# Kernel optimization log

Hardware: AMD Instinct MI355X
Metric: run time of the kernel (lower is better)

The kernel has to match this reference:

```python
import jax, jax.numpy as jnp
import numpy as np

N, E, D_IN, H, NSEG, SEG = 40000, 640000, 127, 128, 512, 64
D0 = D_IN + 1  # node features + batch-indicator column


def setup_inputs() -> dict:
    ks = jax.random.split(jax.random.key(0), 12)
    def w(k, i, o):
        return jax.random.normal(k, (i, o), jnp.float32) / np.float32(np.sqrt(i))
    return dict(
        x=jax.random.normal(ks[0], (N, D_IN), jnp.float32),
        ei=jax.random.randint(ks[1], (2, E), 0, N, jnp.int32),
        ew=jax.random.uniform(ks[2], (E,), jnp.float32),
        batches=jax.random.randint(ks[3], (NSEG * SEG,), 0, N, jnp.int32),
        lens=jnp.arange(NSEG + 1, dtype=jnp.int32) * SEG,  # CSR offsets, 512 segments of 64
        gin_w0=w(ks[4], D0, H), gin_b0=jnp.zeros((H,), jnp.float32),
        gin_w1=w(ks[5], H, H), gin_b1=jnp.zeros((H,), jnp.float32),
        gin_w2=w(ks[6], H, H), gin_b2=jnp.zeros((H,), jnp.float32),
        r_w1=w(ks[7], 3 * H, H), r_b1=jnp.zeros((H,), jnp.float32),
        ln1_g=jnp.ones((H,), jnp.float32), ln1_b=jnp.zeros((H,), jnp.float32),
        r_w2=w(ks[8], H, H), r_b2=jnp.zeros((H,), jnp.float32),
        ln2_g=jnp.ones((H,), jnp.float32), ln2_b=jnp.zeros((H,), jnp.float32),
        r_w3=w(ks[9], H, 1), r_b3=jnp.zeros((1,), jnp.float32),
    )


def _layernorm(v, g, b, eps=1e-5):
    m = jnp.mean(v, -1, keepdims=True)
    var = jnp.mean((v - m) ** 2, -1, keepdims=True)
    return (v - m) * jax.lax.rsqrt(var + eps) * g + b


def _gin_layer(h, src, dst, ew, w, b):
    # GINConv with eps=0: MLP((1+eps)*h + sum_{j->i} ew_ji * h_j), MLP = Linear+ReLU
    agg = jax.ops.segment_sum(ew[:, None] * h[src], dst, num_segments=N)
    return jax.nn.relu((h + agg) @ w + b)


def reference(x, ei, ew, batches, lens,
              gin_w0, gin_b0, gin_w1, gin_b1, gin_w2, gin_b2,
              r_w1, r_b1, ln1_g, ln1_b, r_w2, r_b2, ln2_g, ln2_b, r_w3, r_b3):
    src, dst = ei[0], ei[1]
    # batch indicator feature
    bf = jnp.zeros((N, 1), x.dtype).at[batches].set(1.0)
    h = jnp.concatenate([x, bf], axis=1)  # [N, D0]
    for w_, b_ in ((gin_w0, gin_b0), (gin_w1, gin_b1), (gin_w2, gin_b2)):
        h = _gin_layer(h, src, dst, ew, w_, b_)
    # MultiPool: gather per-subgraph nodes then mean/min/max segment reductions
    seg = jnp.searchsorted(lens, jnp.arange(NSEG * SEG, dtype=jnp.int32), side='right') - 1
    src_e = h[batches]  # [total, H]
    counts = (lens[1:] - lens[:-1]).astype(h.dtype)[:, None]
    mean_p = jax.ops.segment_sum(src_e, seg, num_segments=NSEG) / counts
    min_p = jax.ops.segment_min(src_e, seg, num_segments=NSEG)
    max_p = jax.ops.segment_max(src_e, seg, num_segments=NSEG)
    z = jnp.concatenate([mean_p, min_p, max_p], axis=1)  # [NSEG, 3H]
    # readout: Linear, ReLU, LN, Linear, LN, ReLU, Linear
    z = _layernorm(jax.nn.relu(z @ r_w1 + r_b1), ln1_g, ln1_b)
    z = jax.nn.relu(_layernorm(z @ r_w2 + r_b2, ln2_g, ln2_b))
    return z @ r_w3 + r_b3  # logits [NSEG, 1]
```

## Files before the change

kernel.cpp:

```cpp
#include <hip/hip_runtime.h>
#include <hip/hip_fp16.h>

#define NN   40000
#define EE   640000
#define DIN  127
#define HH   128
#define NSEGS 512
#define SEGSZ 64
#define CAP  64
#define NB_ELL 625
#define NB_H0  10000

typedef unsigned int uint;
typedef unsigned short ushort;
typedef _Float16 f16;
typedef __attribute__((ext_vector_type(8))) _Float16 f16x8;
typedef __attribute__((ext_vector_type(4))) float f32x4;

__device__ __forceinline__ float h2f_lo(uint v) {
    __half_raw r; r.x = (ushort)(v & 0xffff); return __half2float(__half(r));
}
__device__ __forceinline__ float h2f_hi(uint v) {
    __half_raw r; r.x = (ushort)(v >> 16); return __half2float(__half(r));
}
__device__ __forceinline__ ushort f2h(float f) {
    return __half_as_ushort(__float2half(f));
}

__global__ __launch_bounds__(256) void prep(int4* __restrict__ cnt4,
                                            const float* __restrict__ w0,
                                            const float* __restrict__ w1,
                                            const float* __restrict__ w2,
                                            ushort* __restrict__ wp) {
    int t = blockIdx.x * 256 + threadIdx.x;
    if (t < NN * 4) cnt4[t] = make_int4(0, 0, 0, 0);
    if (t < 3 * HH * HH) {
        int l = t / (HH * HH);
        int r = t - l * (HH * HH);
        int n = r >> 7, k = r & 127;
        const float* w = (l == 0) ? w0 : (l == 1) ? w1 : w2;
        wp[t] = f2h(w[k * HH + n]);
    }
}

__global__ __launch_bounds__(256) void ell_h0(const int* __restrict__ ei,
                                              const float* __restrict__ ew,
                                              int* __restrict__ cnt,
                                              uint* __restrict__ ell,
                                              const float* __restrict__ x,
                                              uint* __restrict__ h) {
    int b = blockIdx.x;
    if (b < NB_ELL) {
        int e = (b * 256 + threadIdx.x) * 4;
        int d0 = ei[EE + e + 0], d1 = ei[EE + e + 1];
        int d2 = ei[EE + e + 2], d3 = ei[EE + e + 3];
        int s0 = ei[e + 0], s1 = ei[e + 1], s2 = ei[e + 2], s3 = ei[e + 3];
        float w0 = ew[e + 0], w1 = ew[e + 1], w2 = ew[e + 2], w3 = ew[e + 3];
        int a0 = atomicAdd(&cnt[d0 << 4], 1);
        int a1 = atomicAdd(&cnt[d1 << 4], 1);
        int a2 = atomicAdd(&cnt[d2 << 4], 1);
        int a3 = atomicAdd(&cnt[d3 << 4], 1);
        if (a0 < CAP) ell[(size_t)d0 * CAP + a0] = (uint)s0 | ((uint)f2h(w0) << 16);
        if (a1 < CAP) ell[(size_t)d1 * CAP + a1] = (uint)s1 | ((uint)f2h(w1) << 16);
        if (a2 < CAP) ell[(size_t)d2 * CAP + a2] = (uint)s2 | ((uint)f2h(w2) << 16);
        if (a3 < CAP) ell[(size_t)d3 * CAP + a3] = (uint)s3 | ((uint)f2h(w3) << 16);
    } else {
        int t = (b - NB_ELL) * 256 + threadIdx.x;
        int i = t >> 6, q = t & 63;
        int d0 = q << 1;
        float a = x[i * DIN + d0];
        float bb = (d0 + 1 < DIN) ? x[i * DIN + d0 + 1] : 0.f;
        h[t] = (uint)f2h(a) | ((uint)f2h(bb) << 16);
    }
}

__global__ void set_bf(const int* __restrict__ batches, ushort* __restrict__ h) {
    int j = blockIdx.x * 256 + threadIdx.x;
    if (j < NSEGS * SEGSZ) h[(size_t)batches[j] * HH + DIN] = 0x3C00;
}

__global__ __launch_bounds__(256) void gin_layer(const uint* __restrict__ h,
                                                 const int* __restrict__ cnt,
                                                 const uint* __restrict__ ell,
                                                 const ushort* __restrict__ wp,
                                                 const float* __restrict__ bias,
                                                 ushort* __restrict__ hout) {
    __shared__ __align__(16) uint lds[16 * 64];
    int tid = threadIdx.x;
    int wave = tid >> 6, lane = tid & 63;
    int half = lane >> 5, l32 = lane & 31;

#pragma unroll
    for (int it = 0; it < 2; ++it) {
        int ni = it * 8 + wave * 2 + half;
        int node = blockIdx.x * 16 + ni;
        int n = cnt[node << 4];
        if (n > CAP) n = CAP;
        const uint* row = ell + (size_t)node * CAP;
        uint2 self = *(const uint2*)(h + (size_t)node * 64 + l32 * 2);
        float ax = h2f_lo(self.x), ay = h2f_hi(self.x);
        float az = h2f_lo(self.y), aw = h2f_hi(self.y);
        float bx = 0.f, by = 0.f, bz = 0.f, bw = 0.f;
        int p = 0;
        for (; p + 4 <= n; p += 4) {
            uint4 ee = *(const uint4*)(row + p);
            uint2 v0 = *(const uint2*)(h + (size_t)(ee.x & 0xffff) * 64 + l32 * 2);
            uint2 v1 = *(const uint2*)(h + (size_t)(ee.y & 0xffff) * 64 + l32 * 2);
            uint2 v2 = *(const uint2*)(h + (size_t)(ee.z & 0xffff) * 64 + l32 * 2);
            uint2 v3 = *(const uint2*)(h + (size_t)(ee.w & 0xffff) * 64 + l32 * 2);
            float w0 = h2f_hi(ee.x), w1 = h2f_hi(ee.y);
            float w2 = h2f_hi(ee.z), w3 = h2f_hi(ee.w);
            ax += w0 * h2f_lo(v0.x); ay += w0 * h2f_hi(v0.x);
            az += w0 * h2f_lo(v0.y); aw += w0 * h2f_hi(v0.y);
            bx += w1 * h2f_lo(v1.x); by += w1 * h2f_hi(v1.x);
            bz += w1 * h2f_lo(v1.y); bw += w1 * h2f_hi(v1.y);
            ax += w2 * h2f_lo(v2.x); ay += w2 * h2f_hi(v2.x);
            az += w2 * h2f_lo(v2.y); aw += w2 * h2f_hi(v2.y);
            bx += w3 * h2f_lo(v3.x); by += w3 * h2f_hi(v3.x);
            bz += w3 * h2f_lo(v3.y); bw += w3 * h2f_hi(v3.y);
        }
        for (; p < n; ++p) {
            uint e = row[p];
            float w = h2f_hi(e);
            uint2 v = *(const uint2*)(h + (size_t)(e & 0xffff) * 64 + l32 * 2);
            ax += w * h2f_lo(v.x); ay += w * h2f_hi(v.x);
            az += w * h2f_lo(v.y); aw += w * h2f_hi(v.y);
        }
        ax += bx; ay += by; az += bz; aw += bw;
        uint2 o;
        o.x = (uint)f2h(ax) | ((uint)f2h(ay) << 16);
        o.y = (uint)f2h(az) | ((uint)f2h(aw) << 16);
        int wsw = (l32 * 2) ^ ((ni & 7) << 2);
        *(uint2*)(&lds[ni * 64 + wsw]) = o;
    }
    __syncthreads();

    int n16 = lane & 15, kg = lane >> 4;
    f16x8 a[4];
#pragma unroll
    for (int s = 0; s < 4; ++s) {
        int w = (s * 16 + kg * 4) ^ ((n16 & 7) << 2);
        a[s] = *(const f16x8*)(&lds[n16 * 64 + w]);
    }
    int row0 = blockIdx.x * 16;
#pragma unroll
    for (int t = 0; t < 2; ++t) {
        int ct = wave * 2 + t;
        const f16* brow = (const f16*)wp + (size_t)(ct * 16 + n16) * HH + kg * 8;
        f16x8 b0 = *(const f16x8*)(brow + 0);
        f16x8 b1 = *(const f16x8*)(brow + 32);
        f16x8 b2 = *(const f16x8*)(brow + 64);
        f16x8 b3 = *(const f16x8*)(brow + 96);
        f32x4 c = {0.f, 0.f, 0.f, 0.f};
        c = __builtin_amdgcn_mfma_f32_16x16x32_f16(a[0], b0, c, 0, 0, 0);
        c = __builtin_amdgcn_mfma_f32_16x16x32_f16(a[1], b1, c, 0, 0, 0);
        c = __builtin_amdgcn_mfma_f32_16x16x32_f16(a[2], b2, c, 0, 0, 0);
        c = __builtin_amdgcn_mfma_f32_16x16x32_f16(a[3], b3, c, 0, 0, 0);
        float bv = bias[ct * 16 + n16];
#pragma unroll
        for (int j = 0; j < 4; j++) {
            float o = fmaxf(c[j] + bv, 0.f);
            hout[(size_t)(row0 + kg * 4 + j) * HH + ct * 16 + n16] = f2h(o);
        }
    }
}

__device__ __forceinline__ float block_sum(float v, float* red, int c) {
    red[c] = v;
    __syncthreads();
#pragma unroll
    for (int off = 64; off > 0; off >>= 1) {
        if (c < off) red[c] += red[c + off];
        __syncthreads();
    }
    float r = red[0];
    __syncthreads();
    return r;
}

__global__ __launch_bounds__(128) void pool_readout(const ushort* __restrict__ h,
    const int* __restrict__ batches,
    const float* __restrict__ w1, const float* __restrict__ b1,
    const float* __restrict__ g1, const float* __restrict__ be1,
    const float* __restrict__ w2, const float* __restrict__ b2,
    const float* __restrict__ g2, const float* __restrict__ be2,
    const float* __restrict__ w3, const float* __restrict__ b3,
    float* __restrict__ out) {
    __shared__ float zr[384];
    __shared__ float red[128];
    __shared__ float v1[128];
    int s = blockIdx.x, c = threadIdx.x;

    float sum = 0.f, mn = INFINITY, mx = -INFINITY;
    for (int j = 0; j < SEGSZ; j++) {
        int idx = batches[s * SEGSZ + j];
        __half_raw r; r.x = h[(size_t)idx * HH + c];
        float v = __half2float(__half(r));
        sum += v;
        mn = fminf(mn, v);
        mx = fmaxf(mx, v);
    }
    zr[c] = sum * (1.f / SEGSZ);
    zr[128 + c] = mn;
    zr[256 + c] = mx;
    __syncthreads();

    float a = b1[c];
    for (int k = 0; k < 384; k++) a += zr[k] * w1[k * HH + c];
    a = fmaxf(a, 0.f);
    float m = block_sum(a, red, c) * (1.f / HH);
    float d = a - m;
    float var = block_sum(d * d, red, c) * (1.f / HH);
    float v = d * rsqrtf(var + 1e-5f) * g1[c] + be1[c];
    v1[c] = v;
    __syncthreads();

    float a2 = b2[c];
    for (int k = 0; k < HH; k++) a2 += v1[k] * w2[k * HH + c];
    float m2 = block_sum(a2, red, c) * (1.f / HH);
    float d2 = a2 - m2;
    float var2 = block_sum(d2 * d2, red, c) * (1.f / HH);
    float t2 = d2 * rsqrtf(var2 + 1e-5f) * g2[c] + be2[c];
    float z2 = fmaxf(t2, 0.f);

    float tot = block_sum(z2 * w3[c], red, c);
    if (c == 0) out[s] = tot + b3[0];
}

extern "C" void kernel_launch(void* const* d_in, const int* in_sizes, int n_in,
                              void* d_out, int out_size, void* d_ws, size_t ws_size,
                              hipStream_t stream) {
    const float* x        = (const float*)d_in[0];
    const int*   ei       = (const int*)d_in[1];
    const float* ew       = (const float*)d_in[2];
    const int*   batches  = (const int*)d_in[3];
    const float* gw[3]    = {(const float*)d_in[5], (const float*)d_in[7], (const float*)d_in[9]};
    const float* gb[3]    = {(const float*)d_in[6], (const float*)d_in[8], (const float*)d_in[10]};
    const float* r_w1 = (const float*)d_in[11]; const float* r_b1 = (const float*)d_in[12];
    const float* ln1g = (const float*)d_in[13]; const float* ln1b = (const float*)d_in[14];
    const float* r_w2 = (const float*)d_in[15]; const float* r_b2 = (const float*)d_in[16];
    const float* ln2g = (const float*)d_in[17]; const float* ln2b = (const float*)d_in[18];
    const float* r_w3 = (const float*)d_in[19]; const float* r_b3 = (const float*)d_in[20];
    float* out = (float*)d_out;

    uint*  h0   = (uint*)d_ws;
    uint*  h1   = h0 + (size_t)NN * 64;
    uint*  wpk  = h1 + (size_t)NN * 64;
    uint*  ell  = wpk + 3 * HH * HH / 2;
    int*   cnt  = (int*)(ell + (size_t)NN * CAP);

    prep<<<625, 256, 0, stream>>>((int4*)cnt, gw[0], gw[1], gw[2], (ushort*)wpk);
    ell_h0<<<NB_ELL + NB_H0, 256, 0, stream>>>(ei, ew, cnt, ell, x, h0);
    set_bf<<<(NSEGS * SEGSZ + 255) / 256, 256, 0, stream>>>(batches, (ushort*)h0);

    uint* hin = h0;
    uint* hout = h1;
    for (int l = 0; l < 3; l++) {
        gin_layer<<<NN / 16, 256, 0, stream>>>(hin, cnt, ell,
                                               (const ushort*)wpk + (size_t)l * HH * HH,
                                               gb[l], (ushort*)hout);
        uint* tmp = hin; hin = hout; hout = tmp;
    }

    pool_readout<<<NSEGS, 128, 0, stream>>>((const ushort*)hin, batches,
                                            r_w1, r_b1, ln1g, ln1b,
                                            r_w2, r_b2, ln2g, ln2b, r_w3, r_b3, out);
}
```

Before: 185.3 us.

## Build ELL adjacency via two-pass bucket partition instead of global atomics

Replaces the per-edge global atomic slot allocation into the ELL structure with a two-pass scheme. First, blocks bin edges into 80 buckets of 512 destination nodes using LDS histograms and write them coalesced to a staging region. Then one block per bucket builds ELL rows with LDS atomics and writes the counts. This drops the zeroing of the 40000-entry padded count array and folds set_bf into the second kernel, removing one launch. The cost is an extra round trip through the staging buffer, a fixed per-bucket capacity (RCAP) that silently drops edges beyond it, and only 80 blocks doing the ELL scatter.

```diff
diff --git a/kernel.cpp b/kernel.cpp
--- a/kernel.cpp
+++ b/kernel.cpp
@@ -8,8 +8,10 @@
 #define NSEGS 512
 #define SEGSZ 64
 #define CAP  64
-#define NB_ELL 625
-#define NB_H0  10000
+#define NBUK 80
+#define RCAP 16384
+#define NB_PA 625
+#define NB_H0 10000
 
 typedef unsigned int uint;
 typedef unsigned short ushort;
@@ -27,13 +29,13 @@
     return __half_as_ushort(__float2half(f));
 }
 
-__global__ __launch_bounds__(256) void prep(int4* __restrict__ cnt4,
+__global__ __launch_bounds__(256) void prep(int* __restrict__ gcnt,
                                             const float* __restrict__ w0,
                                             const float* __restrict__ w1,
                                             const float* __restrict__ w2,
                                             ushort* __restrict__ wp) {
     int t = blockIdx.x * 256 + threadIdx.x;
-    if (t < NN * 4) cnt4[t] = make_int4(0, 0, 0, 0);
+    if (t < NBUK) gcnt[t] = 0;
     if (t < 3 * HH * HH) {
         int l = t / (HH * HH);
         int r = t - l * (HH * HH);
@@ -43,40 +45,96 @@
     }
 }
 
-__global__ __launch_bounds__(256) void ell_h0(const int* __restrict__ ei,
-                                              const float* __restrict__ ew,
-                                              int* __restrict__ cnt,
-                                              uint* __restrict__ ell,
-                                              const float* __restrict__ x,
-                                              uint* __restrict__ h) {
+__global__ __launch_bounds__(256) void part_h0(const int* __restrict__ ei,
+                                               const float* __restrict__ ew,
+                                               int* __restrict__ gcnt,
+                                               uint2* __restrict__ region,
+                                               const float* __restrict__ x,
+                                               uint* __restrict__ h) {
+    __shared__ int hist[NBUK];
+    __shared__ int lbase[NBUK];
+    __shared__ int gposs[NBUK];
+    __shared__ uint2 ord[1024];
+    __shared__ uint adrs[1024];
     int b = blockIdx.x;
-    if (b < NB_ELL) {
-        int e = (b * 256 + threadIdx.x) * 4;
-        int d0 = ei[EE + e + 0], d1 = ei[EE + e + 1];
-        int d2 = ei[EE + e + 2], d3 = ei[EE + e + 3];
-        int s0 = ei[e + 0], s1 = ei[e + 1], s2 = ei[e + 2], s3 = ei[e + 3];
-        float w0 = ew[e + 0], w1 = ew[e + 1], w2 = ew[e + 2], w3 = ew[e + 3];
-        int a0 = atomicAdd(&cnt[d0 << 4], 1);
-        int a1 = atomicAdd(&cnt[d1 << 4], 1);
-        int a2 = atomicAdd(&cnt[d2 << 4], 1);
-        int a3 = atomicAdd(&cnt[d3 << 4], 1);
-        if (a0 < CAP) ell[(size_t)d0 * CAP + a0] = (uint)s0 | ((uint)f2h(w0) << 16);
-        if (a1 < CAP) ell[(size_t)d1 * CAP + a1] = (uint)s1 | ((uint)f2h(w1) << 16);
-        if (a2 < CAP) ell[(size_t)d2 * CAP + a2] = (uint)s2 | ((uint)f2h(w2) << 16);
-        if (a3 < CAP) ell[(size_t)d3 * CAP + a3] = (uint)s3 | ((uint)f2h(w3) << 16);
+    int t = threadIdx.x;
+    if (b < NB_PA) {
+        for (int i = t; i < NBUK; i += 256) hist[i] = 0;
+        __syncthreads();
+        int e0 = (b * 256 + t) * 4;
+        int4 ss = *(const int4*)(ei + e0);
+        int4 dd = *(const int4*)(ei + EE + e0);
+        float4 ww = *(const float4*)(ew + e0);
+        int d[4] = {dd.x, dd.y, dd.z, dd.w};
+        int s[4] = {ss.x, ss.y, ss.z, ss.w};
+        float w[4] = {ww.x, ww.y, ww.z, ww.w};
+        int bk[4], loc[4];
+#pragma unroll
+        for (int i = 0; i < 4; i++) {
+            bk[i] = d[i] >> 9;
+            loc[i] = atomicAdd(&hist[bk[i]], 1);
+        }
+        __syncthreads();
+        if (t == 0) {
+            int run = 0;
+            for (int i = 0; i < NBUK; i++) { lbase[i] = run; run += hist[i]; }
+        }
+        if (t < NBUK && hist[t] > 0) gposs[t] = atomicAdd(&gcnt[t], hist[t]);
+        __syncthreads();
+#pragma unroll
+        for (int i = 0; i < 4; i++) {
+            int pos = lbase[bk[i]] + loc[i];
+            ord[pos] = make_uint2((uint)s[i] | ((uint)f2h(w[i]) << 16), (uint)d[i]);
+            int off = gposs[bk[i]] + loc[i];
+            adrs[pos] = (off < RCAP) ? (uint)(bk[i] * RCAP + off) : 0xFFFFFFFFu;
+        }
+        __syncthreads();
+        for (int idx = t; idx < 1024; idx += 256) {
+            uint a = adrs[idx];
+            if (a != 0xFFFFFFFFu) region[a] = ord[idx];
+        }
     } else {
-        int t = (b - NB_ELL) * 256 + threadIdx.x;
-        int i = t >> 6, q = t & 63;
+        int tt = (b - NB_PA) * 256 + t;
+        int i = tt >> 6, q = tt & 63;
         int d0 = q << 1;
         float a = x[i * DIN + d0];
         float bb = (d0 + 1 < DIN) ? x[i * DIN + d0 + 1] : 0.f;
-        h[t] = (uint)f2h(a) | ((uint)f2h(bb) << 16);
-    }
-}
-
-__global__ void set_bf(const int* __restrict__ batches, ushort* __restrict__ h) {
-    int j = blockIdx.x * 256 + threadIdx.x;
-    if (j < NSEGS * SEGSZ) h[(size_t)batches[j] * HH + DIN] = 0x3C00;
+        h[tt] = (uint)f2h(a) | ((uint)f2h(bb) << 16);
+    }
+}
+
+__global__ __launch_bounds__(256) void ellb_setbf(const uint2* __restrict__ region,
+                                                  const int* __restrict__ gcnt,
+                                                  uint* __restrict__ ell,
+                                                  int* __restrict__ cnt,
+                                                  const int* __restrict__ batches,
+                                                  ushort* __restrict__ h) {
+    int b = blockIdx.x;
+    int t = threadIdx.x;
+    if (b < NBUK) {
+        __shared__ int lc[512];
+        lc[t] = 0; lc[t + 256] = 0;
+        __syncthreads();
+        int n = gcnt[b];
+        if (n > RCAP) n = RCAP;
+        const uint2* reg = region + (size_t)b * RCAP;
+        for (int i = t; i < n; i += 256) {
+            uint2 r = reg[i];
+            int d = (int)r.y;
+            int slot = atomicAdd(&lc[d & 511], 1);
+            if (slot < CAP) ell[(size_t)d * CAP + slot] = r.x;
+        }
+        __syncthreads();
+        int node0 = b << 9;
+#pragma unroll
+        for (int i = 0; i < 2; i++) {
+            int node = node0 + t + i * 256;
+            if (node < NN) cnt[node << 4] = lc[t + i * 256];
+        }
+    } else {
+        int j = (b - NBUK) * 256 + t;
+        if (j < NSEGS * SEGSZ) h[(size_t)batches[j] * HH + DIN] = 0x3C00;
+    }
 }
 
 __global__ __launch_bounds__(256) void gin_layer(const uint* __restrict__ h,
@@ -243,15 +301,17 @@
     const float* r_w3 = (const float*)d_in[19]; const float* r_b3 = (const float*)d_in[20];
     float* out = (float*)d_out;
 
-    uint*  h0   = (uint*)d_ws;
-    uint*  h1   = h0 + (size_t)NN * 64;
-    uint*  wpk  = h1 + (size_t)NN * 64;
-    uint*  ell  = wpk + 3 * HH * HH / 2;
-    int*   cnt  = (int*)(ell + (size_t)NN * CAP);
-
-    prep<<<625, 256, 0, stream>>>((int4*)cnt, gw[0], gw[1], gw[2], (ushort*)wpk);
-    ell_h0<<<NB_ELL + NB_H0, 256, 0, stream>>>(ei, ew, cnt, ell, x, h0);
-    set_bf<<<(NSEGS * SEGSZ + 255) / 256, 256, 0, stream>>>(batches, (ushort*)h0);
+    uint*  h0     = (uint*)d_ws;
+    uint*  h1     = h0 + (size_t)NN * 64;
+    uint*  wpk    = h1 + (size_t)NN * 64;
+    uint*  ell    = wpk + 3 * HH * HH / 2;
+    int*   cnt    = (int*)(ell + (size_t)NN * CAP);
+    uint2* region = (uint2*)(cnt + (size_t)NN * 16);
+    int*   gcnt   = (int*)(region + (size_t)NBUK * RCAP);
+
+    prep<<<192, 256, 0, stream>>>(gcnt, gw[0], gw[1], gw[2], (ushort*)wpk);
+    part_h0<<<NB_PA + NB_H0, 256, 0, stream>>>(ei, ew, gcnt, region, x, h0);
+    ellb_setbf<<<NBUK + 128, 256, 0, stream>>>(region, gcnt, ell, cnt, batches, (ushort*)h0);
 
     uint* hin = h0;
     uint* hout = h1;
```

Result: faster. 179.7 us (-3.0%).
